# Performance work log

Hardware: AMD Instinct MI355X
Metric: run time of the kernel (lower is better)

## Reference

```python
import math
import jax, jax.numpy as jnp
import numpy as np

B, T, D, M, S = 2, 4096, 1024, 256, 8
BEAM = 4
TAU = 1.0


def setup_inputs() -> dict:
    key = jax.random.key(0)
    ks = jax.random.split(key, 24)
    std = 0.02
    inp = {
        "mu": jax.random.normal(ks[0], (B, T, D), jnp.float32),
        "lam": jax.random.uniform(ks[1], (B, T, D), jnp.float32),
        "pi": jax.random.uniform(ks[2], (B, T, 7), jnp.float32),
        "pi_write": jax.random.uniform(ks[3], (B, T, 1), jnp.float32),
        "Wq": jax.random.normal(ks[4], (M, D), jnp.float32) * std,
        "bq": jnp.zeros((M,), jnp.float32),
        "Wk": jax.random.normal(ks[5], (M, D), jnp.float32) * std,
        "bk": jnp.zeros((M,), jnp.float32),
        "Wv": jax.random.normal(ks[6], (M, D), jnp.float32) * std,
        "bv": jnp.zeros((M,), jnp.float32),
        "Wo": jax.random.normal(ks[7], (D, M), jnp.float32) * std,
        "bo": jnp.zeros((D,), jnp.float32),
        "Ws1": jax.random.normal(ks[8], (256, 2 * D + 7), jnp.float32) * std,
        "bs1": jnp.zeros((256,), jnp.float32),
        "Ws2": jax.random.normal(ks[9], (1, 256), jnp.float32) * std,
        "bs2": jnp.zeros((1,), jnp.float32),
        "Wsr": jax.random.normal(ks[10], (M, M), jnp.float32) * std,
        "bsr": jnp.zeros((M,), jnp.float32),
        "scratch_init": jax.random.normal(ks[11], (1, S, M), jnp.float32) * 0.02,
        "gate": jnp.float32(-5.0),
    }
    return inp


def _build_tree(k, v, w):
    """Causal binary tree of weighted span summaries. Level 0 = leaves."""
    levels = [(k, v, w)]
    while k.shape[1] > 1:
        n = k.shape[1]
        if n % 2 == 1:
            pad = ((0, 0), (0, 1), (0, 0))
            k = jnp.pad(k, pad); v = jnp.pad(v, pad); w = jnp.pad(w, pad)
        k1, k2 = k[:, 0::2], k[:, 1::2]
        v1, v2 = v[:, 0::2], v[:, 1::2]
        w1, w2 = w[:, 0::2], w[:, 1::2]
        tw = w1 + w2 + 1e-8
        k = (w1 * k1 + w2 * k2) / tw
        v = (w1 * v1 + w2 * v2) / tw
        w = tw
        levels.append((k, v, w))
    return levels


def _retrieve_at_level(q, keys, values, beam):
    Bq, Tq, Mq = q.shape
    n = keys.shape[1]
    scores = jnp.einsum('btm,bnm->btn', q, keys) / math.sqrt(Mq)
    if n <= Tq:  # causal: query i may only see slot j <= i
        mask = jnp.arange(n)[None, :] > jnp.arange(Tq)[:, None]
        scores = jnp.where(mask[None], -jnp.inf, scores)
    kk = min(beam, n)
    if n > kk:
        vals, idx = jax.lax.top_k(scores, kk)           # (B,T,k)
        p = jax.nn.softmax(vals, axis=-1)               # == softmax of scattered sparse scores
        v_sel = jnp.take_along_axis(values[:, None], idx[..., None], axis=2)  # (B,T,k,M)
        return jnp.einsum('btk,btkm->btm', p, v_sel)
    attn = jax.nn.softmax(scores, axis=-1)
    return jnp.einsum('btn,bnm->btm', attn, values)


def reference(mu, lam, pi, pi_write, Wq, bq, Wk, bk, Wv, bv, Wo, bo,
              Ws1, bs1, Ws2, bs2, Wsr, bsr, scratch_init, gate):
    # ---- write: build causal tree from detached keys/values ----
    mu_d = jax.lax.stop_gradient(mu)
    w0 = jax.lax.stop_gradient(pi_write)                # (B,T,1)
    k = mu_d @ Wk.T + bk
    v = mu_d @ Wv.T + bv
    tree = _build_tree(k, v, w0)

    # ---- read ----
    q = mu @ Wq.T + bq                                  # (B,T,M)
    log_var = -jnp.log(jnp.clip(lam, 1e-6))
    si = jnp.concatenate([mu, log_var, pi], axis=-1)    # (B,T,2D+7)
    h = si @ Ws1.T + bs1
    h = h * jax.nn.sigmoid(h)                           # SiLU
    s = jax.nn.sigmoid((h @ Ws2.T + bs2)[..., 0])       # (B,T)

    scratch = jnp.broadcast_to(scratch_init, (mu.shape[0], S, M))
    sq = q @ Wsr.T + bsr
    sattn = jax.nn.softmax(jnp.einsum('btm,bsm->bts', sq, scratch) / math.sqrt(M), axis=-1)
    scratch_ctx = jnp.einsum('bts,bsm->btm', sattn, scratch)

    level_ctx = [_retrieve_at_level(q, lk, lv, BEAM) for (lk, lv, _) in tree]
    level_stack = jnp.stack(level_ctx, axis=2)          # (B,T,L,M)
    L = level_stack.shape[2]
    level_idx = jnp.arange(L, dtype=mu.dtype)
    s_scaled = s[..., None] * (L - 1)                   # (B,T,1)
    kappa = jnp.exp(-0.5 * ((level_idx - s_scaled) / TAU) ** 2)
    kappa = kappa / jnp.clip(kappa.sum(axis=-1, keepdims=True), 1e-8)
    tree_ctx = jnp.einsum('btl,btlm->btm', kappa, level_stack)

    blend = s[..., None]
    combined = (1.0 - blend) * tree_ctx + blend * scratch_ctx
    out = combined @ Wo.T + bo
    return jax.nn.sigmoid(gate) * out                   # (B,T,D)
```

## Files before the change

### kernel.cpp

```cpp
#include <hip/hip_runtime.h>
#include <math.h>

#define TT 4096
#define BB 2
#define MMDIM 256
#define RTOT 8192
#define NSLICE 39

typedef __attribute__((ext_vector_type(8))) short short8_t;
typedef __attribute__((ext_vector_type(4))) float f32x4;

__device__ __forceinline__ unsigned short f2bf(float x)
{
    unsigned u = __float_as_uint(x);
    u += 0x7fffu + ((u >> 16) & 1u);
    return (unsigned short)(u >> 16);
}

__global__ __launch_bounds__(256) void gemm_qk(
    const float* __restrict__ mu, const float* __restrict__ Wq,
    const float* __restrict__ bq, const float* __restrict__ Wk,
    const float* __restrict__ bk, float* __restrict__ q_, float* __restrict__ k_,
    unsigned short* __restrict__ qkh, unsigned short* __restrict__ qkl)
{
    __shared__ float As[2][8][68];
    __shared__ float Ws[2][8][132];
    const int tid = threadIdx.x;
    const int tx = tid & 15;
    const int ty = tid >> 4;
    const int r0 = blockIdx.x * 64;
    const int c0 = blockIdx.y * 128;
    const bool isq = (c0 < 256);

    const float* W = isq ? (Wq + (size_t)c0 * 1024)
                         : (Wk + (size_t)(c0 - 256) * 1024);
    const float* bias = isq ? (bq + c0) : (bk + (c0 - 256));

    const bool isA = (tid < 128);
    const int sArow = tid >> 1, sAk = (tid & 1) * 4;
    const int sWrow = tid >> 1, sWk = (tid & 1) * 4;

    float acc[4][8] = {};
    float4 rA, rW;

    if (isA) rA = *(const float4*)&mu[(size_t)(r0 + sArow) * 1024 + sAk];
    rW = *(const float4*)&W[(size_t)sWrow * 1024 + sWk];
    if (isA) {
        As[0][sAk + 0][sArow] = rA.x; As[0][sAk + 1][sArow] = rA.y;
        As[0][sAk + 2][sArow] = rA.z; As[0][sAk + 3][sArow] = rA.w;
    }
    Ws[0][sWk + 0][sWrow] = rW.x; Ws[0][sWk + 1][sWrow] = rW.y;
    Ws[0][sWk + 2][sWrow] = rW.z; Ws[0][sWk + 3][sWrow] = rW.w;
    __syncthreads();

    int buf = 0;
    for (int k0 = 0; k0 < 1024; k0 += 8) {
        const bool has = (k0 + 8 < 1024);
        if (has) {
            if (isA) rA = *(const float4*)&mu[(size_t)(r0 + sArow) * 1024 + k0 + 8 + sAk];
            rW = *(const float4*)&W[(size_t)sWrow * 1024 + k0 + 8 + sWk];
        }
        #pragma unroll
        for (int kk = 0; kk < 8; ++kk) {
            float4 a  = *(const float4*)&As[buf][kk][ty * 4];
            float4 b0 = *(const float4*)&Ws[buf][kk][tx * 8];
            float4 b1 = *(const float4*)&Ws[buf][kk][tx * 8 + 4];
            float av[4] = {a.x, a.y, a.z, a.w};
            float bv[8] = {b0.x, b0.y, b0.z, b0.w, b1.x, b1.y, b1.z, b1.w};
            #pragma unroll
            for (int i = 0; i < 4; ++i)
                #pragma unroll
                for (int j = 0; j < 8; ++j)
                    acc[i][j] += av[i] * bv[j];
        }
        if (has) {
            int nb = buf ^ 1;
            if (isA) {
                As[nb][sAk + 0][sArow] = rA.x; As[nb][sAk + 1][sArow] = rA.y;
                As[nb][sAk + 2][sArow] = rA.z; As[nb][sAk + 3][sArow] = rA.w;
            }
            Ws[nb][sWk + 0][sWrow] = rW.x; Ws[nb][sWk + 1][sWrow] = rW.y;
            Ws[nb][sWk + 2][sWrow] = rW.z; Ws[nb][sWk + 3][sWrow] = rW.w;
        }
        __syncthreads();
        buf ^= 1;
    }

    const int lcol = (c0 & 255) + tx * 8;
    #pragma unroll
    for (int i = 0; i < 4; ++i) {
        int row = r0 + ty * 4 + i;
        float o[8];
        #pragma unroll
        for (int j = 0; j < 8; ++j) o[j] = acc[i][j] + bias[tx * 8 + j];
        float* dst = isq ? &q_[(size_t)row * MMDIM + lcol]
                         : &k_[(size_t)row * MMDIM + lcol];
        *(float4*)dst       = make_float4(o[0], o[1], o[2], o[3]);
        *(float4*)(dst + 4) = make_float4(o[4], o[5], o[6], o[7]);
        size_t srow = isq ? (size_t)row : (size_t)(RTOT + row);
        short8_t sh, sl;
        #pragma unroll
        for (int j = 0; j < 8; ++j) {
            unsigned short h = f2bf(o[j]);
            sh[j] = (short)h;
            sl[j] = (short)f2bf(o[j] - __uint_as_float((unsigned)h << 16));
        }
        *(short8_t*)&qkh[srow * MMDIM + lcol] = sh;
        *(short8_t*)&qkl[srow * MMDIM + lcol] = sl;
    }
}

__device__ __forceinline__ void split4(const float* src, unsigned short* hi,
                                       unsigned short* lo, int i)
{
    float4 x = ((const float4*)src)[i];
    ushort4 h, l;
    h.x = f2bf(x.x); l.x = f2bf(x.x - __uint_as_float((unsigned)h.x << 16));
    h.y = f2bf(x.y); l.y = f2bf(x.y - __uint_as_float((unsigned)h.y << 16));
    h.z = f2bf(x.z); l.z = f2bf(x.z - __uint_as_float((unsigned)h.z << 16));
    h.w = f2bf(x.w); l.w = f2bf(x.w - __uint_as_float((unsigned)h.w << 16));
    ((ushort4*)hi)[i] = h;
    ((ushort4*)lo)[i] = l;
}

__global__ __launch_bounds__(256) void split_weights(
    const float* __restrict__ Ws1, const float* __restrict__ Wv,
    const float* __restrict__ Wsr, const float* __restrict__ Wo,
    unsigned short* __restrict__ w1h, unsigned short* __restrict__ w1l,
    unsigned short* __restrict__ wvh, unsigned short* __restrict__ wvl,
    unsigned short* __restrict__ wsrh, unsigned short* __restrict__ wsrl,
    unsigned short* __restrict__ woh, unsigned short* __restrict__ wol)
{
    const int bid = blockIdx.x;
    const int tid = threadIdx.x;
    if (bid < 256) {
        int r = bid;
        for (int c = tid; c < 2112; c += 256) {
            float v = (c < 2055) ? Ws1[(size_t)r * 2055 + c] : 0.f;
            unsigned short h = f2bf(v);
            w1h[(size_t)r * 2112 + c] = h;
            w1l[(size_t)r * 2112 + c] = f2bf(v - __uint_as_float((unsigned)h << 16));
        }
    } else if (bid < 512) {
        split4(Wv, wvh, wvl, (bid - 256) * 256 + tid);
    } else if (bid < 576) {
        split4(Wsr, wsrh, wsrl, (bid - 512) * 256 + tid);
    } else {
        split4(Wo, woh, wol, (bid - 576) * 256 + tid);
    }
}

template<int ASRC, int WITH_GATE>
__global__ __launch_bounds__(256) void gemm_mfma(
    const float* __restrict__ A, const float* __restrict__ lam,
    const float* __restrict__ pi,
    const unsigned short* __restrict__ Wh, const unsigned short* __restrict__ Wl,
    const float* __restrict__ bias, const float* __restrict__ gate,
    float* __restrict__ C, int K, int N)
{
    __shared__ unsigned short Ah[64][72], Al[64][72];
    __shared__ unsigned short Bh[128][72], Bl[128][72];
    const int tid = threadIdx.x;
    const int lane = tid & 63;
    const int wv = tid >> 6;
    const int r0 = blockIdx.x * 64;
    const int c0 = blockIdx.y * 128;

    f32x4 acc0[8] = {}, acc1[8] = {}, acc2[8] = {};

    const int arow = wv * 16 + (lane & 15);
    const int koff = (lane >> 4) * 8;

    for (int kc = 0; kc < K; kc += 64) {
        #pragma unroll
        for (int i = 0; i < 2; ++i) {
            int g = tid + i * 256;
            int row = g >> 3, gq = g & 7;
            float x[8];
            if (ASRC == 0) {
                float4 v0 = *(const float4*)&A[(size_t)(r0 + row) * K + kc + gq * 8];
                float4 v1 = *(const float4*)&A[(size_t)(r0 + row) * K + kc + gq * 8 + 4];
                x[0] = v0.x; x[1] = v0.y; x[2] = v0.z; x[3] = v0.w;
                x[4] = v1.x; x[5] = v1.y; x[6] = v1.z; x[7] = v1.w;
            } else {
                #pragma unroll
                for (int e = 0; e < 8; ++e) {
                    int c = kc + gq * 8 + e;
                    float val;
                    if (c < 1024)      val = A[(size_t)(r0 + row) * 1024 + c];
                    else if (c < 2048) val = -logf(fmaxf(lam[(size_t)(r0 + row) * 1024 + (c - 1024)], 1e-6f));
                    else if (c < 2055) val = pi[(size_t)(r0 + row) * 7 + (c - 2048)];
                    else               val = 0.f;
                    x[e] = val;
                }
            }
            short8_t sh, sl;
            #pragma unroll
            for (int e = 0; e < 8; ++e) {
                unsigned short h = f2bf(x[e]);
                sh[e] = (short)h;
                sl[e] = (short)f2bf(x[e] - __uint_as_float((unsigned)h << 16));
            }
            *(short8_t*)&Ah[row][gq * 8] = sh;
            *(short8_t*)&Al[row][gq * 8] = sl;
        }
        #pragma unroll
        for (int i = 0; i < 4; ++i) {
            int g = tid + i * 256;
            int row = g >> 3, gq = g & 7;
            *(short8_t*)&Bh[row][gq * 8] = *(const short8_t*)&Wh[(size_t)(c0 + row) * K + kc + gq * 8];
            *(short8_t*)&Bl[row][gq * 8] = *(const short8_t*)&Wl[(size_t)(c0 + row) * K + kc + gq * 8];
        }
        __syncthreads();
        #pragma unroll
        for (int kt = 0; kt < 2; ++kt) {
            short8_t afh = *(const short8_t*)&Ah[arow][kt * 32 + koff];
            short8_t afl = *(const short8_t*)&Al[arow][kt * 32 + koff];
            #pragma unroll
            for (int ct = 0; ct < 8; ++ct) {
                short8_t bh = *(const short8_t*)&Bh[ct * 16 + (lane & 15)][kt * 32 + koff];
                short8_t bl = *(const short8_t*)&Bl[ct * 16 + (lane & 15)][kt * 32 + koff];
                acc0[ct] = __builtin_amdgcn_mfma_f32_16x16x32_bf16(afh, bh, acc0[ct], 0, 0, 0);
                acc1[ct] = __builtin_amdgcn_mfma_f32_16x16x32_bf16(afl, bh, acc1[ct], 0, 0, 0);
                acc2[ct] = __builtin_amdgcn_mfma_f32_16x16x32_bf16(afh, bl, acc2[ct], 0, 0, 0);
            }
        }
        __syncthreads();
    }

    float g = 1.f;
    if (WITH_GATE) g = 1.f / (1.f + expf(-gate[0]));
    #pragma unroll
    for (int ct = 0; ct < 8; ++ct) {
        int col = c0 + ct * 16 + (lane & 15);
        float b = bias[col];
        #pragma unroll
        for (int r = 0; r < 4; ++r) {
            int row = r0 + wv * 16 + (lane >> 4) * 4 + r;
            C[(size_t)row * N + col] = (acc0[ct][r] + acc1[ct][r] + acc2[ct][r] + b) * g;
        }
    }
}

__global__ __launch_bounds__(256) void s_scratch_kernel(
    const float* __restrict__ h, const float* __restrict__ Ws2,
    const float* __restrict__ bs2, const float* __restrict__ sq,
    const float* __restrict__ scr, float* __restrict__ kap,
    float* __restrict__ ctx)
{
    const int tid = threadIdx.x;
    const int wave = tid >> 6, lane = tid & 63;
    const int t = blockIdx.x * 4 + wave;

    float4 hv = *(const float4*)&h[(size_t)t * MMDIM + lane * 4];
    float4 wv = *(const float4*)&Ws2[lane * 4];
    float p = 0.f;
    p += (hv.x / (1.f + expf(-hv.x))) * wv.x;
    p += (hv.y / (1.f + expf(-hv.y))) * wv.y;
    p += (hv.z / (1.f + expf(-hv.z))) * wv.z;
    p += (hv.w / (1.f + expf(-hv.w))) * wv.w;
    #pragma unroll
    for (int o = 32; o; o >>= 1) p += __shfl_xor(p, o);

    float z = p + bs2[0];
    float s = 1.f / (1.f + expf(-z));
    float c = s * 12.f;
    float Z = 0.f;
    #pragma unroll
    for (int l = 0; l < 13; ++l) {
        float d = (float)l - c;
        Z += expf(-0.5f * d * d);
    }
    Z = fmaxf(Z, 1e-8f);
    if (lane < 13) {
        float d = (float)lane - c;
        kap[(size_t)t * 16 + lane] = (1.f - s) * expf(-0.5f * d * d) / Z;
    }

    float4 qv = *(const float4*)&sq[(size_t)t * MMDIM + lane * 4];
    float4 fr[8];
    float sc[8];
    #pragma unroll
    for (int ss = 0; ss < 8; ++ss) {
        fr[ss] = *(const float4*)&scr[ss * MMDIM + lane * 4];
        sc[ss] = qv.x * fr[ss].x + qv.y * fr[ss].y + qv.z * fr[ss].z + qv.w * fr[ss].w;
    }
    #pragma unroll
    for (int ss = 0; ss < 8; ++ss) {
        #pragma unroll
        for (int o = 32; o; o >>= 1) sc[ss] += __shfl_xor(sc[ss], o);
        sc[ss] *= 0.0625f;
    }
    float mx = sc[0];
    #pragma unroll
    for (int ss = 1; ss < 8; ++ss) mx = fmaxf(mx, sc[ss]);
    float sum = 0.f;
    #pragma unroll
    for (int ss = 0; ss < 8; ++ss) { sc[ss] = expf(sc[ss] - mx); sum += sc[ss]; }
    float inv = 1.f / sum;
    float4 o = {0, 0, 0, 0};
    #pragma unroll
    for (int ss = 0; ss < 8; ++ss) {
        float pp = sc[ss] * inv;
        o.x += pp * fr[ss].x; o.y += pp * fr[ss].y;
        o.z += pp * fr[ss].z; o.w += pp * fr[ss].w;
    }
    o.x *= s; o.y *= s; o.z *= s; o.w *= s;
    *(float4*)&ctx[(size_t)t * MMDIM + lane * 4] = o;
}

__global__ __launch_bounds__(256) void wtree_kernel(
    const float* __restrict__ pw, float* __restrict__ wtree)
{
    __shared__ float wa[4096];
    __shared__ float wb2[2048];
    const int b = blockIdx.x;
    const int tid = threadIdx.x;
    for (int t = tid; t < 4096; t += 256) wa[t] = pw[b * 4096 + t];
    __syncthreads();
    int n = 4096, lvl = 1;
    float* cur = wa; float* nxt = wb2;
    while (n > 1) {
        int nout = n >> 1;
        int off = TT - (8192 >> lvl);
        for (int j = tid; j < nout; j += 256) {
            float t = cur[2 * j] + cur[2 * j + 1] + 1e-8f;
            nxt[j] = t;
            wtree[b * 4095 + off + j] = t;
        }
        __syncthreads();
        float* tmp = cur; cur = nxt; nxt = tmp;
        n = nout; ++lvl;
    }
}

__global__ __launch_bounds__(256) void tree_all(
    const float* __restrict__ kleaf, const float* __restrict__ vleaf,
    const float* __restrict__ pw, const float* __restrict__ wtree,
    float* __restrict__ kt_, float* __restrict__ vt_,
    unsigned short* __restrict__ kth, unsigned short* __restrict__ ktl)
{
    __shared__ float kb[254][64];
    __shared__ float vb[254][64];
    const int tid = threadIdx.x;
    const int g  = blockIdx.x >> 2;
    const int mc = blockIdx.x & 3;
    const int b  = blockIdx.y;
    const int wb = b * 4095;

    for (int idx = tid; idx < 128 * 64; idx += 256) {
        int j = idx >> 6, m = idx & 63;
        size_t gi = ((size_t)b * TT + g * 128 + j) * MMDIM + mc * 64 + m;
        kb[j][m] = kleaf[gi];
        vb[j][m] = vleaf[gi];
    }
    __syncthreads();

    int pb = 0, cb = 128;
    for (int l = 1; l <= 6; ++l) {
        int nloc = 64 >> (l - 1);
        int offl = TT - (8192 >> l);
        int gbase = g * nloc;
        for (int idx = tid; idx < nloc * 64; idx += 256) {
            int j = idx >> 6, m = idx & 63;
            float w1, w2;
            if (l == 1) {
                w1 = pw[b * 4096 + (gbase + j) * 2];
                w2 = pw[b * 4096 + (gbase + j) * 2 + 1];
            } else {
                int offm1 = TT - (8192 >> (l - 1));
                w1 = wtree[wb + offm1 + (gbase + j) * 2];
                w2 = wtree[wb + offm1 + (gbase + j) * 2 + 1];
            }
            float tw = wtree[wb + offl + gbase + j];
            float kvv = (w1 * kb[pb + 2 * j][m] + w2 * kb[pb + 2 * j + 1][m]) / tw;
            float vvv = (w1 * vb[pb + 2 * j][m] + w2 * vb[pb + 2 * j + 1][m]) / tw;
            kb[cb + j][m] = kvv;
            vb[cb + j][m] = vvv;
            size_t go = (size_t)(wb + offl + gbase + j) * MMDIM + mc * 64 + m;
            kt_[go] = kvv;
            vt_[go] = vvv;
            unsigned short hh = f2bf(kvv);
            kth[go] = hh;
            ktl[go] = f2bf(kvv - __uint_as_float((unsigned)hh << 16));
        }
        __syncthreads();
        pb = cb; cb += nloc;
    }
}

__global__ __launch_bounds__(256) void tree_deep(
    float* __restrict__ kt_, float* __restrict__ vt_,
    const float* __restrict__ wtree,
    unsigned short* __restrict__ kth, unsigned short* __restrict__ ktl)
{
    __shared__ float kb[128][68];
    __shared__ float vb[128][68];
    const int tid = threadIdx.x;
    const int mc = blockIdx.x;
    const int b = blockIdx.y;
    const int wb = b * 4095;

    for (int idx = tid; idx < 64 * 64; idx += 256) {
        int j = idx >> 6, m = idx & 63;
        size_t gi = (size_t)(wb + 3968 + j) * MMDIM + mc * 64 + m;
        kb[j][m] = kt_[gi];
        vb[j][m] = vt_[gi];
    }
    __syncthreads();

    int pb = 0;
    for (int l = 7; l <= 12; ++l) {
        int nout = 4096 >> l;
        int cb = 128 - (128 >> (l - 6));
        int offm1 = TT - (8192 >> (l - 1));
        int offl  = TT - (8192 >> l);
        for (int idx = tid; idx < nout * 64; idx += 256) {
            int j = idx >> 6, m = idx & 63;
            float w1 = wtree[wb + offm1 + 2 * j];
            float w2 = wtree[wb + offm1 + 2 * j + 1];
            float tw = wtree[wb + offl + j];
            float kvv = (w1 * kb[pb + 2 * j][m] + w2 * kb[pb + 2 * j + 1][m]) / tw;
            float vvv = (w1 * vb[pb + 2 * j][m] + w2 * vb[pb + 2 * j + 1][m]) / tw;
            kb[cb + j][m] = kvv;
            vb[cb + j][m] = vvv;
            size_t go = (size_t)(wb + offl + j) * MMDIM + mc * 64 + m;
            kt_[go] = kvv;
            vt_[go] = vvv;
            unsigned short hh = f2bf(kvv);
            kth[go] = hh;
            ktl[go] = f2bf(kvv - __uint_as_float((unsigned)hh << 16));
        }
        __syncthreads();
        pb = cb;
    }
}

__device__ __forceinline__ unsigned long long pack_key(float v, int col)
{
    unsigned u = __float_as_uint(v);
    u ^= ((unsigned)((int)u >> 31)) | 0x80000000u;
    return ((unsigned long long)u << 32) | (unsigned)(~col);
}

__device__ __forceinline__ void unpack_key(unsigned long long k, float& v, int& col)
{
    unsigned u = (unsigned)(k >> 32);
    u ^= (u & 0x80000000u) ? 0x80000000u : 0xFFFFFFFFu;
    v = __uint_as_float(u);
    col = (int)(~(unsigned)k);
}

__device__ __forceinline__ unsigned long long shfl_xor_u64(unsigned long long v, int off)
{
    int lo = __shfl_xor((int)(unsigned)v, off);
    int hi = __shfl_xor((int)(v >> 32), off);
    return ((unsigned long long)(unsigned)hi << 32) | (unsigned)lo;
}

__device__ __forceinline__ void ins4u(unsigned long long k, unsigned long long t[4])
{
    if (k <= t[3]) return;
    t[3] = k;
    if (t[3] > t[2]) { unsigned long long x = t[2]; t[2] = t[3]; t[3] = x; }
    if (t[2] > t[1]) { unsigned long long x = t[1]; t[1] = t[2]; t[2] = x; }
    if (t[1] > t[0]) { unsigned long long x = t[0]; t[0] = t[1]; t[1] = x; }
}

__device__ __forceinline__ void ins5u(unsigned long long k, unsigned long long t[5])
{
    if (k <= t[4]) return;
    t[4] = k;
    if (t[4] > t[3]) { unsigned long long x = t[3]; t[3] = t[4]; t[4] = x; }
    if (t[3] > t[2]) { unsigned long long x = t[2]; t[2] = t[3]; t[3] = x; }
    if (t[2] > t[1]) { unsigned long long x = t[1]; t[1] = t[2]; t[2] = x; }
    if (t[1] > t[0]) { unsigned long long x = t[0]; t[0] = t[1]; t[1] = x; }
}

__device__ __forceinline__ bool beats(float v, int id, float v2, int id2)
{
    return (v > v2) || (v == v2 && id < id2);
}

__device__ __forceinline__ void ins5(float v, int id, float tv[5], int ti[5])
{
    if (!beats(v, id, tv[4], ti[4])) return;
    tv[4] = v; ti[4] = id;
    #pragma unroll
    for (int s = 4; s > 0; --s) {
        if (beats(tv[s], ti[s], tv[s - 1], ti[s - 1])) {
            float fv = tv[s]; tv[s] = tv[s - 1]; tv[s - 1] = fv;
            int iv = ti[s]; ti[s] = ti[s - 1]; ti[s - 1] = iv;
        }
    }
}

__device__ __forceinline__ void slice_map(int sid, int& level, int& c0)
{
    if (sid < 16)      { level = 0; c0 = sid << 8; }
    else if (sid < 24) { level = 1; c0 = (sid - 16) << 8; }
    else if (sid < 28) { level = 2; c0 = (sid - 24) << 8; }
    else if (sid < 30) { level = 3; c0 = (sid - 28) << 8; }
    else               { level = sid - 26; c0 = 0; }
}

__global__ __launch_bounds__(256) void topk_mfma(
    const unsigned short* __restrict__ qkh, const unsigned short* __restrict__ qkl,
    const unsigned short* __restrict__ kth, const unsigned short* __restrict__ ktl,
    float2* __restrict__ topw)
{
    __shared__ unsigned short kbh[32][264];
    __shared__ unsigned short kbl[32][264];

    const int tid = threadIdx.x;
    const int lane = tid & 63;
    const int wv = tid >> 6;
    const int r0 = blockIdx.x * 64;
    const int sid = blockIdx.y;
    const int b = r0 >> 12;
    const int t0 = r0 & 4095;

    int level, c0b;
    slice_map(sid, level, c0b);
    const int n = TT >> level;
    const int nv = min(min(n, t0 + 64), c0b + 256);

    if (c0b >= nv) {
        if (tid < 64) {
            float2 e = make_float2(-INFINITY, __int_as_float(0x7fffffff));
            #pragma unroll
            for (int s = 0; s < 5; ++s)
                topw[(size_t)(sid * 5 + s) * RTOT + r0 + tid] = e;
        }
        return;
    }

    const unsigned short* Kh;
    const unsigned short* Kl;
    if (level == 0) {
        Kh = qkh + (size_t)RTOT * MMDIM + (size_t)b * TT * MMDIM;
        Kl = qkl + (size_t)RTOT * MMDIM + (size_t)b * TT * MMDIM;
    } else {
        size_t off = (size_t)b * 4095 + (TT - (8192 >> level));
        Kh = kth + off * MMDIM;
        Kl = ktl + off * MMDIM;
    }

    const int arow = r0 + wv * 16 + (lane & 15);
    const int koff = (lane >> 4) * 8;
    short8_t ah[8], al[8];
    #pragma unroll
    for (int kt = 0; kt < 8; ++kt) {
        ah[kt] = *(const short8_t*)(qkh + (size_t)arow * MMDIM + kt * 32 + koff);
        al[kt] = *(const short8_t*)(qkl + (size_t)arow * MMDIM + kt * 32 + koff);
    }

    unsigned long long tk[4][4] = {};
    const int trow0 = t0 + wv * 16 + (lane >> 4) * 4;

    const int scol = tid >> 3;
    const int kseg = (tid & 7) * 32;

    for (int c0 = c0b; c0 < nv; c0 += 32) {
        {
            int cc = min(c0 + scol, n - 1);
            const unsigned short* gh = Kh + (size_t)cc * MMDIM + kseg;
            const unsigned short* gl = Kl + (size_t)cc * MMDIM + kseg;
            #pragma unroll
            for (int i = 0; i < 4; ++i) {
                *(short8_t*)&kbh[scol][kseg + i * 8] = *(const short8_t*)(gh + i * 8);
                *(short8_t*)&kbl[scol][kseg + i * 8] = *(const short8_t*)(gl + i * 8);
            }
        }
        __syncthreads();

        #pragma unroll
        for (int ct = 0; ct < 2; ++ct) {
            f32x4 a0 = {0.f, 0.f, 0.f, 0.f};
            f32x4 a1 = {0.f, 0.f, 0.f, 0.f};
            f32x4 a2 = {0.f, 0.f, 0.f, 0.f};
            const int bc = ct * 16 + (lane & 15);
            #pragma unroll
            for (int kt = 0; kt < 8; ++kt) {
                short8_t bh = *(const short8_t*)&kbh[bc][kt * 32 + koff];
                short8_t bl = *(const short8_t*)&kbl[bc][kt * 32 + koff];
                a0 = __builtin_amdgcn_mfma_f32_16x16x32_bf16(ah[kt], bh, a0, 0, 0, 0);
                a1 = __builtin_amdgcn_mfma_f32_16x16x32_bf16(al[kt], bh, a1, 0, 0, 0);
                a2 = __builtin_amdgcn_mfma_f32_16x16x32_bf16(ah[kt], bl, a2, 0, 0, 0);
            }
            const int col = c0 + bc;
            #pragma unroll
            for (int r = 0; r < 4; ++r) {
                float sc = (a0[r] + a1[r] + a2[r]) * 0.0625f;
                unsigned long long key =
                    (col <= trow0 + r && col < n) ? pack_key(sc, col) : 0ull;
                if (__any(key > tk[r][3])) ins4u(key, tk[r]);
            }
        }
        __syncthreads();
    }

    #pragma unroll
    for (int r = 0; r < 4; ++r) {
        unsigned long long k5[5];
        #pragma unroll
        for (int s = 0; s < 4; ++s) k5[s] = tk[r][s];
        k5[4] = 0ull;
        #pragma unroll
        for (int pass = 0; pass < 4; ++pass) {
            int off = 1 << pass;
            unsigned long long o[5];
            #pragma unroll
            for (int s = 0; s < 5; ++s) o[s] = shfl_xor_u64(k5[s], off);
            #pragma unroll
            for (int s = 0; s < 5; ++s) ins5u(o[s], k5);
        }
        if ((lane & 15) == 0) {
            int row = r0 + wv * 16 + (lane >> 4) * 4 + r;
            #pragma unroll
            for (int s = 0; s < 5; ++s) {
                float2 e;
                if (k5[s] == 0ull) {
                    e = make_float2(-INFINITY, __int_as_float(0x7fffffff));
                } else {
                    float v; int c;
                    unpack_key(k5[s], v, c);
                    e = make_float2(v, __int_as_float(c));
                }
                topw[(size_t)(sid * 5 + s) * RTOT + row] = e;
            }
        }
    }
}

__global__ __launch_bounds__(256) void merge_gather(
    const float2* __restrict__ topw, const float* __restrict__ q,
    const float* __restrict__ kl0, const float* __restrict__ ktf,
    const float* __restrict__ vl0, const float* __restrict__ vtree,
    const float* __restrict__ kap, float* __restrict__ ctx)
{
    const int tid = threadIdx.x;
    const int lane = tid & 63;
    const int wv = __builtin_amdgcn_readfirstlane(tid >> 6);
    const int row = blockIdx.x * 4 + wv;
    const int b = row >> 12;

    float cr[4] = {0, 0, 0, 0};
    const float4 q4 = *(const float4*)&q[(size_t)row * MMDIM + lane * 4];

    for (int l = 0; l <= 12; ++l) {
        int s0, cnt;
        if (l == 0)      { s0 = 0;  cnt = 16; }
        else if (l == 1) { s0 = 16; cnt = 8; }
        else if (l == 2) { s0 = 24; cnt = 4; }
        else if (l == 3) { s0 = 28; cnt = 2; }
        else             { s0 = 26 + l; cnt = 1; }

        float tv[5]; int ti[5];
        #pragma unroll
        for (int s = 0; s < 5; ++s) { tv[s] = -INFINITY; ti[s] = 0x7fffffff; }
        for (int sl = 0; sl < cnt; ++sl) {
            #pragma unroll
            for (int s = 0; s < 5; ++s) {
                float2 e = topw[(size_t)((s0 + sl) * 5 + s) * RTOT + row];
                if (e.x > -INFINITY) ins5(e.x, __float_as_int(e.y), tv, ti);
            }
        }

        const float* Kf = (l == 0)
            ? kl0 + (size_t)b * TT * MMDIM
            : ktf + ((size_t)b * 4095 + (TT - (8192 >> l))) * MMDIM;

        bool ambig = (l <= 9) && (tv[3] - tv[4] < 1e-4f);
        if (ambig) {
            float rv[5]; int ri[5];
            #pragma unroll
            for (int s = 0; s < 5; ++s) { rv[s] = -INFINITY; ri[s] = 0x7fffffff; }
            for (int sl = 0; sl < cnt; ++sl) {
                #pragma unroll
                for (int s = 0; s < 5; ++s) {
                    float2 e = topw[(size_t)((s0 + sl) * 5 + s) * RTOT + row];
                    if (e.x > -INFINITY) {
                        int idx = __float_as_int(e.y);
                        float4 k4 = *(const float4*)&Kf[(size_t)idx * MMDIM + lane * 4];
                        float p = q4.x * k4.x + q4.y * k4.y + q4.z * k4.z + q4.w * k4.w;
                        #pragma unroll
                        for (int o = 32; o; o >>= 1) p += __shfl_xor(p, o);
                        ins5(p * 0.0625f, idx, rv, ri);
                    }
                }
            }
            #pragma unroll
            for (int s = 0; s < 5; ++s) { tv[s] = rv[s]; ti[s] = ri[s]; }
        }

        float m0 = tv[0];
        float e0 = expf(tv[0] - m0);
        float e1 = expf(tv[1] - m0);
        float e2 = expf(tv[2] - m0);
        float e3 = expf(tv[3] - m0);
        float sum = e0 + e1 + e2 + e3;
        float kp = kap[(size_t)row * 16 + l];
        float scl = kp / sum;
        float ps[4] = {e0 * scl, e1 * scl, e2 * scl, e3 * scl};

        const float* Vb = (l == 0)
            ? vl0 + (size_t)b * TT * MMDIM
            : vtree + ((size_t)b * 4095 + (TT - (8192 >> l))) * MMDIM;

        #pragma unroll
        for (int s = 0; s < 4; ++s) {
            if (ps[s] > 0.f) {
                float4 vv = *(const float4*)&Vb[(size_t)ti[s] * MMDIM + lane * 4];
                cr[0] += ps[s] * vv.x; cr[1] += ps[s] * vv.y;
                cr[2] += ps[s] * vv.z; cr[3] += ps[s] * vv.w;
            }
        }
    }

    float* cp = ctx + (size_t)row * MMDIM + lane * 4;
    float4 c = *(float4*)cp;
    c.x += cr[0]; c.y += cr[1]; c.z += cr[2]; c.w += cr[3];
    *(float4*)cp = c;
}

extern "C" void kernel_launch(void* const* d_in, const int* in_sizes, int n_in,
                              void* d_out, int out_size, void* d_ws, size_t ws_size,
                              hipStream_t stream)
{
    const float* mu  = (const float*)d_in[0];
    const float* lam = (const float*)d_in[1];
    const float* pi  = (const float*)d_in[2];
    const float* pw  = (const float*)d_in[3];
    const float* Wq  = (const float*)d_in[4];
    const float* bq  = (const float*)d_in[5];
    const float* Wk  = (const float*)d_in[6];
    const float* bk  = (const float*)d_in[7];
    const float* Wv  = (const float*)d_in[8];
    const float* bv  = (const float*)d_in[9];
    const float* Wo  = (const float*)d_in[10];
    const float* bo  = (const float*)d_in[11];
    const float* Ws1 = (const float*)d_in[12];
    const float* bs1 = (const float*)d_in[13];
    const float* Ws2 = (const float*)d_in[14];
    const float* bs2 = (const float*)d_in[15];
    const float* Wsr = (const float*)d_in[16];
    const float* bsr = (const float*)d_in[17];
    const float* scr = (const float*)d_in[18];
    const float* gate = (const float*)d_in[19];
    float* out = (float*)d_out;

    float* w = (float*)d_ws;
    const size_t RM = (size_t)RTOT * MMDIM;
    float* q_   = w;  w += RM;
    float* k_   = w;  w += RM;
    float* v_   = w;  w += RM;
    float* h_   = w;  w += RM;
    float* sq_  = w;  w += RM;
    float* ctx_ = w;  w += RM;
    float* sb_  = w;  w += RTOT;
    float* kap_ = w;  w += (size_t)RTOT * 16;
    float* kt_  = w;  w += (size_t)BB * 4095 * MMDIM;
    float* vt_  = w;  w += (size_t)BB * 4095 * MMDIM;
    float* wtree_ = w; w += (size_t)BB * 4095;
    unsigned short* qkh_ = (unsigned short*)w;  w += RM;
    unsigned short* qkl_ = (unsigned short*)w;  w += RM;
    unsigned short* kth_ = (unsigned short*)w;  w += (size_t)BB * 4095 * MMDIM / 2;
    unsigned short* ktl_ = (unsigned short*)w;  w += (size_t)BB * 4095 * MMDIM / 2;
    float2* topw = (float2*)w;  w += (size_t)NSLICE * 5 * RTOT * 2;
    unsigned short* w1h_ = (unsigned short*)w;  w += (size_t)256 * 2112 / 2;
    unsigned short* w1l_ = (unsigned short*)w;  w += (size_t)256 * 2112 / 2;
    unsigned short* wvh_ = (unsigned short*)w;  w += (size_t)256 * 1024 / 2;
    unsigned short* wvl_ = (unsigned short*)w;  w += (size_t)256 * 1024 / 2;
    unsigned short* wsrh_ = (unsigned short*)w; w += (size_t)256 * 256 / 2;
    unsigned short* wsrl_ = (unsigned short*)w; w += (size_t)256 * 256 / 2;
    unsigned short* woh_ = (unsigned short*)w;  w += (size_t)1024 * 256 / 2;
    unsigned short* wol_ = (unsigned short*)w;  w += (size_t)1024 * 256 / 2;
    (void)sb_;

    split_weights<<<832, 256, 0, stream>>>(Ws1, Wv, Wsr, Wo,
                                           w1h_, w1l_, wvh_, wvl_,
                                           wsrh_, wsrl_, woh_, wol_);

    gemm_qk<<<dim3(128, 4), 256, 0, stream>>>(mu, Wq, bq, Wk, bk,
                                              q_, k_, qkh_, qkl_);
    gemm_mfma<0, 0><<<dim3(128, 2), 256, 0, stream>>>(mu, nullptr, nullptr, wvh_, wvl_,
                                                      bv, nullptr, v_, 1024, 256);
    gemm_mfma<1, 0><<<dim3(128, 2), 256, 0, stream>>>(mu, lam, pi, w1h_, w1l_,
                                                      bs1, nullptr, h_, 2112, 256);
    gemm_mfma<0, 0><<<dim3(128, 2), 256, 0, stream>>>(q_, nullptr, nullptr, wsrh_, wsrl_,
                                                      bsr, nullptr, sq_, 256, 256);
    s_scratch_kernel<<<2048, 256, 0, stream>>>(h_, Ws2, bs2, sq_, scr, kap_, ctx_);

    wtree_kernel<<<BB, 256, 0, stream>>>(pw, wtree_);
    tree_all<<<dim3(128, BB), 256, 0, stream>>>(k_, v_, pw, wtree_, kt_, vt_,
                                                kth_, ktl_);
    tree_deep<<<dim3(4, BB), 256, 0, stream>>>(kt_, vt_, wtree_, kth_, ktl_);

    topk_mfma<<<dim3(128, NSLICE), 256, 0, stream>>>(qkh_, qkl_, kth_, ktl_, topw);
    merge_gather<<<2048, 256, 0, stream>>>(topw, q_, k_, kt_, v_, vt_, kap_, ctx_);
    gemm_mfma<0, 1><<<dim3(128, 8), 256, 0, stream>>>(ctx_, nullptr, nullptr, woh_, wol_,
                                                      bo, gate, out, 256, 1024);
}
```

Baseline: 735.1 us.

## Fuse QK GEMM with weight splitting, merge V/H GEMMs, compute tree weights in-block

Folds the weight bf16 hi/lo splitting into the Q/K projection kernel as extra blocks, retiled to 128 threads with an 8x8 per-thread micro-tile. Merges the V and H MFMA GEMMs into one launch selected by blockIdx.y. Drops the separate tree-weight kernel: tree_all and tree_deep now build the per-level weights in shared memory, and only level-6 weights pass between them. This removes several kernel launches and serial small-grid work, at the cost of larger per-thread register use in the QK GEMM and mixed block roles.

```diff
diff --git a/kernel.cpp b/kernel.cpp
--- a/kernel.cpp
+++ b/kernel.cpp
@@ -15,99 +15,6 @@
     unsigned u = __float_as_uint(x);
     u += 0x7fffu + ((u >> 16) & 1u);
     return (unsigned short)(u >> 16);
-}
-
-__global__ __launch_bounds__(256) void gemm_qk(
-    const float* __restrict__ mu, const float* __restrict__ Wq,
-    const float* __restrict__ bq, const float* __restrict__ Wk,
-    const float* __restrict__ bk, float* __restrict__ q_, float* __restrict__ k_,
-    unsigned short* __restrict__ qkh, unsigned short* __restrict__ qkl)
-{
-    __shared__ float As[2][8][68];
-    __shared__ float Ws[2][8][132];
-    const int tid = threadIdx.x;
-    const int tx = tid & 15;
-    const int ty = tid >> 4;
-    const int r0 = blockIdx.x * 64;
-    const int c0 = blockIdx.y * 128;
-    const bool isq = (c0 < 256);
-
-    const float* W = isq ? (Wq + (size_t)c0 * 1024)
-                         : (Wk + (size_t)(c0 - 256) * 1024);
-    const float* bias = isq ? (bq + c0) : (bk + (c0 - 256));
-
-    const bool isA = (tid < 128);
-    const int sArow = tid >> 1, sAk = (tid & 1) * 4;
-    const int sWrow = tid >> 1, sWk = (tid & 1) * 4;
-
-    float acc[4][8] = {};
-    float4 rA, rW;
-
-    if (isA) rA = *(const float4*)&mu[(size_t)(r0 + sArow) * 1024 + sAk];
-    rW = *(const float4*)&W[(size_t)sWrow * 1024 + sWk];
-    if (isA) {
-        As[0][sAk + 0][sArow] = rA.x; As[0][sAk + 1][sArow] = rA.y;
-        As[0][sAk + 2][sArow] = rA.z; As[0][sAk + 3][sArow] = rA.w;
-    }
-    Ws[0][sWk + 0][sWrow] = rW.x; Ws[0][sWk + 1][sWrow] = rW.y;
-    Ws[0][sWk + 2][sWrow] = rW.z; Ws[0][sWk + 3][sWrow] = rW.w;
-    __syncthreads();
-
-    int buf = 0;
-    for (int k0 = 0; k0 < 1024; k0 += 8) {
-        const bool has = (k0 + 8 < 1024);
-        if (has) {
-            if (isA) rA = *(const float4*)&mu[(size_t)(r0 + sArow) * 1024 + k0 + 8 + sAk];
-            rW = *(const float4*)&W[(size_t)sWrow * 1024 + k0 + 8 + sWk];
-        }
-        #pragma unroll
-        for (int kk = 0; kk < 8; ++kk) {
-            float4 a  = *(const float4*)&As[buf][kk][ty * 4];
-            float4 b0 = *(const float4*)&Ws[buf][kk][tx * 8];
-            float4 b1 = *(const float4*)&Ws[buf][kk][tx * 8 + 4];
-            float av[4] = {a.x, a.y, a.z, a.w};
-            float bv[8] = {b0.x, b0.y, b0.z, b0.w, b1.x, b1.y, b1.z, b1.w};
-            #pragma unroll
-            for (int i = 0; i < 4; ++i)
-                #pragma unroll
-                for (int j = 0; j < 8; ++j)
-                    acc[i][j] += av[i] * bv[j];
-        }
-        if (has) {
-            int nb = buf ^ 1;
-            if (isA) {
-                As[nb][sAk + 0][sArow] = rA.x; As[nb][sAk + 1][sArow] = rA.y;
-                As[nb][sAk + 2][sArow] = rA.z; As[nb][sAk + 3][sArow] = rA.w;
-            }
-            Ws[nb][sWk + 0][sWrow] = rW.x; Ws[nb][sWk + 1][sWrow] = rW.y;
-            Ws[nb][sWk + 2][sWrow] = rW.z; Ws[nb][sWk + 3][sWrow] = rW.w;
-        }
-        __syncthreads();
-        buf ^= 1;
-    }
-
-    const int lcol = (c0 & 255) + tx * 8;
-    #pragma unroll
-    for (int i = 0; i < 4; ++i) {
-        int row = r0 + ty * 4 + i;
-        float o[8];
-        #pragma unroll
-        for (int j = 0; j < 8; ++j) o[j] = acc[i][j] + bias[tx * 8 + j];
-        float* dst = isq ? &q_[(size_t)row * MMDIM + lcol]
-                         : &k_[(size_t)row * MMDIM + lcol];
-        *(float4*)dst       = make_float4(o[0], o[1], o[2], o[3]);
-        *(float4*)(dst + 4) = make_float4(o[4], o[5], o[6], o[7]);
-        size_t srow = isq ? (size_t)row : (size_t)(RTOT + row);
-        short8_t sh, sl;
-        #pragma unroll
-        for (int j = 0; j < 8; ++j) {
-            unsigned short h = f2bf(o[j]);
-            sh[j] = (short)h;
-            sl[j] = (short)f2bf(o[j] - __uint_as_float((unsigned)h << 16));
-        }
-        *(short8_t*)&qkh[srow * MMDIM + lcol] = sh;
-        *(short8_t*)&qkl[srow * MMDIM + lcol] = sl;
-    }
 }
 
 __device__ __forceinline__ void split4(const float* src, unsigned short* hi,
@@ -123,7 +30,11 @@
     ((ushort4*)lo)[i] = l;
 }
 
-__global__ __launch_bounds__(256) void split_weights(
+__global__ __launch_bounds__(128) void qk_split(
+    const float* __restrict__ mu, const float* __restrict__ Wq,
+    const float* __restrict__ bq, const float* __restrict__ Wk,
+    const float* __restrict__ bk, float* __restrict__ q_, float* __restrict__ k_,
+    unsigned short* __restrict__ qkh, unsigned short* __restrict__ qkl,
     const float* __restrict__ Ws1, const float* __restrict__ Wv,
     const float* __restrict__ Wsr, const float* __restrict__ Wo,
     unsigned short* __restrict__ w1h, unsigned short* __restrict__ w1l,
@@ -131,40 +42,140 @@
     unsigned short* __restrict__ wsrh, unsigned short* __restrict__ wsrl,
     unsigned short* __restrict__ woh, unsigned short* __restrict__ wol)
 {
+    __shared__ float As[2][8][68];
+    __shared__ float Ws[2][8][132];
     const int bid = blockIdx.x;
     const int tid = threadIdx.x;
-    if (bid < 256) {
-        int r = bid;
-        for (int c = tid; c < 2112; c += 256) {
-            float v = (c < 2055) ? Ws1[(size_t)r * 2055 + c] : 0.f;
-            unsigned short h = f2bf(v);
-            w1h[(size_t)r * 2112 + c] = h;
-            w1l[(size_t)r * 2112 + c] = f2bf(v - __uint_as_float((unsigned)h << 16));
-        }
-    } else if (bid < 512) {
-        split4(Wv, wvh, wvl, (bid - 256) * 256 + tid);
-    } else if (bid < 576) {
-        split4(Wsr, wsrh, wsrl, (bid - 512) * 256 + tid);
-    } else {
-        split4(Wo, woh, wol, (bid - 576) * 256 + tid);
+
+    if (bid >= 512) {
+        const int sid = bid - 512;
+        if (sid < 256) {
+            int r = sid;
+            for (int c = tid; c < 2112; c += 128) {
+                float v = (c < 2055) ? Ws1[(size_t)r * 2055 + c] : 0.f;
+                unsigned short h = f2bf(v);
+                w1h[(size_t)r * 2112 + c] = h;
+                w1l[(size_t)r * 2112 + c] = f2bf(v - __uint_as_float((unsigned)h << 16));
+            }
+        } else if (sid < 768) {
+            split4(Wv, wvh, wvl, (sid - 256) * 128 + tid);
+        } else if (sid < 896) {
+            split4(Wsr, wsrh, wsrl, (sid - 768) * 128 + tid);
+        } else {
+            split4(Wo, woh, wol, (sid - 896) * 128 + tid);
+        }
+        return;
+    }
+
+    const int bx = bid >> 2;
+    const int by = bid & 3;
+    const int r0 = bx * 64;
+    const int c0 = by * 128;
+    const bool isq = (c0 < 256);
+
+    const float* W = isq ? (Wq + (size_t)c0 * 1024)
+                         : (Wk + (size_t)(c0 - 256) * 1024);
+    const float* bias = isq ? (bq + (c0 & 255)) : (bk + (c0 & 255));
+
+    const int tx = tid & 15;
+    const int ty = tid >> 4;
+    const int sArow = tid >> 1, sAk = (tid & 1) * 4;
+    const int sWcol = tid;
+
+    float acc[8][8] = {};
+    float4 rA, rW0, rW1;
+
+    rA  = *(const float4*)&mu[(size_t)(r0 + sArow) * 1024 + sAk];
+    rW0 = *(const float4*)&W[(size_t)sWcol * 1024 + 0];
+    rW1 = *(const float4*)&W[(size_t)sWcol * 1024 + 4];
+    As[0][sAk + 0][sArow] = rA.x; As[0][sAk + 1][sArow] = rA.y;
+    As[0][sAk + 2][sArow] = rA.z; As[0][sAk + 3][sArow] = rA.w;
+    Ws[0][0][sWcol] = rW0.x; Ws[0][1][sWcol] = rW0.y;
+    Ws[0][2][sWcol] = rW0.z; Ws[0][3][sWcol] = rW0.w;
+    Ws[0][4][sWcol] = rW1.x; Ws[0][5][sWcol] = rW1.y;
+    Ws[0][6][sWcol] = rW1.z; Ws[0][7][sWcol] = rW1.w;
+    __syncthreads();
+
+    int buf = 0;
+    for (int k0 = 0; k0 < 1024; k0 += 8) {
+        const bool has = (k0 + 8 < 1024);
+        if (has) {
+            rA  = *(const float4*)&mu[(size_t)(r0 + sArow) * 1024 + k0 + 8 + sAk];
+            rW0 = *(const float4*)&W[(size_t)sWcol * 1024 + k0 + 8];
+            rW1 = *(const float4*)&W[(size_t)sWcol * 1024 + k0 + 12];
+        }
+        #pragma unroll
+        for (int kk = 0; kk < 8; ++kk) {
+            float4 a0 = *(const float4*)&As[buf][kk][ty * 4];
+            float4 a1 = *(const float4*)&As[buf][kk][32 + ty * 4];
+            float4 b0 = *(const float4*)&Ws[buf][kk][tx * 4];
+            float4 b1 = *(const float4*)&Ws[buf][kk][64 + tx * 4];
+            float av[8] = {a0.x, a0.y, a0.z, a0.w, a1.x, a1.y, a1.z, a1.w};
+            float bv[8] = {b0.x, b0.y, b0.z, b0.w, b1.x, b1.y, b1.z, b1.w};
+            #pragma unroll
+            for (int i = 0; i < 8; ++i)
+                #pragma unroll
+                for (int j = 0; j < 8; ++j)
+                    acc[i][j] += av[i] * bv[j];
+        }
+        if (has) {
+            int nb = buf ^ 1;
+            As[nb][sAk + 0][sArow] = rA.x; As[nb][sAk + 1][sArow] = rA.y;
+            As[nb][sAk + 2][sArow] = rA.z; As[nb][sAk + 3][sArow] = rA.w;
+            Ws[nb][0][sWcol] = rW0.x; Ws[nb][1][sWcol] = rW0.y;
+            Ws[nb][2][sWcol] = rW0.z; Ws[nb][3][sWcol] = rW0.w;
+            Ws[nb][4][sWcol] = rW1.x; Ws[nb][5][sWcol] = rW1.y;
+            Ws[nb][6][sWcol] = rW1.z; Ws[nb][7][sWcol] = rW1.w;
+        }
+        __syncthreads();
+        buf ^= 1;
+    }
+
+    const int lc0 = (c0 & 255) + tx * 4;
+    const int lc1 = lc0 + 64;
+    #pragma unroll
+    for (int i = 0; i < 8; ++i) {
+        int row = r0 + ((i < 4) ? (ty * 4 + i) : (32 + ty * 4 + i - 4));
+        float o[8];
+        #pragma unroll
+        for (int j = 0; j < 4; ++j) o[j]     = acc[i][j]     + bias[tx * 4 + j];
+        #pragma unroll
+        for (int j = 0; j < 4; ++j) o[4 + j] = acc[i][4 + j] + bias[64 + tx * 4 + j];
+        float* dst = isq ? q_ : k_;
+        *(float4*)&dst[(size_t)row * MMDIM + lc0] = make_float4(o[0], o[1], o[2], o[3]);
+        *(float4*)&dst[(size_t)row * MMDIM + lc1] = make_float4(o[4], o[5], o[6], o[7]);
+        size_t srow = isq ? (size_t)row : (size_t)(RTOT + row);
+        ushort4 h0, l0, h1, l1;
+        h0.x = f2bf(o[0]); l0.x = f2bf(o[0] - __uint_as_float((unsigned)h0.x << 16));
+        h0.y = f2bf(o[1]); l0.y = f2bf(o[1] - __uint_as_float((unsigned)h0.y << 16));
+        h0.z = f2bf(o[2]); l0.z = f2bf(o[2] - __uint_as_float((unsigned)h0.z << 16));
+        h0.w = f2bf(o[3]); l0.w = f2bf(o[3] - __uint_as_float((unsigned)h0.w << 16));
+        h1.x = f2bf(o[4]); l1.x = f2bf(o[4] - __uint_as_float((unsigned)h1.x << 16));
+        h1.y = f2bf(o[5]); l1.y = f2bf(o[5] - __uint_as_float((unsigned)h1.y << 16));
+        h1.z = f2bf(o[6]); l1.z = f2bf(o[6] - __uint_as_float((unsigned)h1.z << 16));
+        h1.w = f2bf(o[7]); l1.w = f2bf(o[7] - __uint_as_float((unsigned)h1.w << 16));
+        *(ushort4*)&qkh[srow * MMDIM + lc0] = h0;
+        *(ushort4*)&qkl[srow * MMDIM + lc0] = l0;
+        *(ushort4*)&qkh[srow * MMDIM + lc1] = h1;
+        *(ushort4*)&qkl[srow * MMDIM + lc1] = l1;
     }
 }
 
 template<int ASRC, int WITH_GATE>
-__global__ __launch_bounds__(256) void gemm_mfma(
+__device__ __forceinline__ void gemm_mfma_body(
+    unsigned short (*Ah)[72], unsigned short (*Al)[72],
+    unsigned short (*Bh)[72], unsigned short (*Bl)[72],
     const float* __restrict__ A, const float* __restrict__ lam,
     const float* __restrict__ pi,
     const unsigned short* __restrict__ Wh, const unsigned short* __restrict__ Wl,
     const float* __restrict__ bias, const float* __restrict__ gate,
-    float* __restrict__ C, int K, int N)
-{
-    __shared__ unsigned short Ah[64][72], Al[64][72];
-    __shared__ unsigned short Bh[128][72], Bl[128][72];
+    float* __restrict__ C, int K, int N, int bx, int by)
+{
     const int tid = threadIdx.x;
     const int lane = tid & 63;
     const int wv = tid >> 6;
-    const int r0 = blockIdx.x * 64;
-    const int c0 = blockIdx.y * 128;
+    const int r0 = bx * 64;
+    const int c0 = by * 128;
 
     f32x4 acc0[8] = {}, acc1[8] = {}, acc2[8] = {};
 
@@ -242,6 +253,39 @@
     }
 }
 
+template<int ASRC, int WITH_GATE>
+__global__ __launch_bounds__(256) void gemm_mfma(
+    const float* __restrict__ A, const float* __restrict__ lam,
+    const float* __restrict__ pi,
+    const unsigned short* __restrict__ Wh, const unsigned short* __restrict__ Wl,
+    const float* __restrict__ bias, const float* __restrict__ gate,
+    float* __restrict__ C, int K, int N)
+{
+    __shared__ unsigned short Ah[64][72], Al[64][72];
+    __shared__ unsigned short Bh[128][72], Bl[128][72];
+    gemm_mfma_body<ASRC, WITH_GATE>(Ah, Al, Bh, Bl, A, lam, pi, Wh, Wl,
+                                    bias, gate, C, K, N, blockIdx.x, blockIdx.y);
+}
+
+__global__ __launch_bounds__(256) void gemm_vh(
+    const float* __restrict__ mu, const float* __restrict__ lam,
+    const float* __restrict__ pi,
+    const unsigned short* __restrict__ wvh, const unsigned short* __restrict__ wvl,
+    const float* __restrict__ bv,
+    const unsigned short* __restrict__ w1h, const unsigned short* __restrict__ w1l,
+    const float* __restrict__ bs1,
+    float* __restrict__ v_, float* __restrict__ h_)
+{
+    __shared__ unsigned short Ah[64][72], Al[64][72];
+    __shared__ unsigned short Bh[128][72], Bl[128][72];
+    if (blockIdx.y < 2)
+        gemm_mfma_body<0, 0>(Ah, Al, Bh, Bl, mu, nullptr, nullptr, wvh, wvl,
+                             bv, nullptr, v_, 1024, 256, blockIdx.x, blockIdx.y);
+    else
+        gemm_mfma_body<1, 0>(Ah, Al, Bh, Bl, mu, lam, pi, w1h, w1l,
+                             bs1, nullptr, h_, 2112, 256, blockIdx.x, blockIdx.y - 2);
+}
+
 __global__ __launch_bounds__(256) void s_scratch_kernel(
     const float* __restrict__ h, const float* __restrict__ Ws2,
     const float* __restrict__ bs2, const float* __restrict__ sq,
@@ -309,39 +353,15 @@
     *(float4*)&ctx[(size_t)t * MMDIM + lane * 4] = o;
 }
 
-__global__ __launch_bounds__(256) void wtree_kernel(
-    const float* __restrict__ pw, float* __restrict__ wtree)
-{
-    __shared__ float wa[4096];
-    __shared__ float wb2[2048];
-    const int b = blockIdx.x;
-    const int tid = threadIdx.x;
-    for (int t = tid; t < 4096; t += 256) wa[t] = pw[b * 4096 + t];
-    __syncthreads();
-    int n = 4096, lvl = 1;
-    float* cur = wa; float* nxt = wb2;
-    while (n > 1) {
-        int nout = n >> 1;
-        int off = TT - (8192 >> lvl);
-        for (int j = tid; j < nout; j += 256) {
-            float t = cur[2 * j] + cur[2 * j + 1] + 1e-8f;
-            nxt[j] = t;
-            wtree[b * 4095 + off + j] = t;
-        }
-        __syncthreads();
-        float* tmp = cur; cur = nxt; nxt = tmp;
-        n = nout; ++lvl;
-    }
-}
-
 __global__ __launch_bounds__(256) void tree_all(
     const float* __restrict__ kleaf, const float* __restrict__ vleaf,
-    const float* __restrict__ pw, const float* __restrict__ wtree,
+    const float* __restrict__ pw, float* __restrict__ wl6,
     float* __restrict__ kt_, float* __restrict__ vt_,
     unsigned short* __restrict__ kth, unsigned short* __restrict__ ktl)
 {
     __shared__ float kb[254][64];
     __shared__ float vb[254][64];
+    __shared__ float wl[254];
     const int tid = threadIdx.x;
     const int g  = blockIdx.x >> 2;
     const int mc = blockIdx.x & 3;
@@ -354,25 +374,22 @@
         kb[j][m] = kleaf[gi];
         vb[j][m] = vleaf[gi];
     }
+    if (tid < 128) wl[tid] = pw[b * 4096 + g * 128 + tid];
     __syncthreads();
 
     int pb = 0, cb = 128;
     for (int l = 1; l <= 6; ++l) {
-        int nloc = 64 >> (l - 1);
+        int nloc = 128 >> l;
         int offl = TT - (8192 >> l);
         int gbase = g * nloc;
+        if (tid < nloc)
+            wl[cb + tid] = wl[pb + 2 * tid] + wl[pb + 2 * tid + 1] + 1e-8f;
+        __syncthreads();
         for (int idx = tid; idx < nloc * 64; idx += 256) {
             int j = idx >> 6, m = idx & 63;
-            float w1, w2;
-            if (l == 1) {
-                w1 = pw[b * 4096 + (gbase + j) * 2];
-                w2 = pw[b * 4096 + (gbase + j) * 2 + 1];
-            } else {
-                int offm1 = TT - (8192 >> (l - 1));
-                w1 = wtree[wb + offm1 + (gbase + j) * 2];
-                w2 = wtree[wb + offm1 + (gbase + j) * 2 + 1];
-            }
-            float tw = wtree[wb + offl + gbase + j];
+            float w1 = wl[pb + 2 * j];
+            float w2 = wl[pb + 2 * j + 1];
+            float tw = wl[cb + j];
             float kvv = (w1 * kb[pb + 2 * j][m] + w2 * kb[pb + 2 * j + 1][m]) / tw;
             float vvv = (w1 * vb[pb + 2 * j][m] + w2 * vb[pb + 2 * j + 1][m]) / tw;
             kb[cb + j][m] = kvv;
@@ -387,15 +404,17 @@
         __syncthreads();
         pb = cb; cb += nloc;
     }
+    if (mc == 0 && tid < 2) wl6[b * 64 + g * 2 + tid] = wl[pb + tid];
 }
 
 __global__ __launch_bounds__(256) void tree_deep(
     float* __restrict__ kt_, float* __restrict__ vt_,
-    const float* __restrict__ wtree,
+    const float* __restrict__ wl6,
     unsigned short* __restrict__ kth, unsigned short* __restrict__ ktl)
 {
     __shared__ float kb[128][68];
     __shared__ float vb[128][68];
+    __shared__ float wl[127];
     const int tid = threadIdx.x;
     const int mc = blockIdx.x;
     const int b = blockIdx.y;
@@ -407,19 +426,23 @@
         kb[j][m] = kt_[gi];
         vb[j][m] = vt_[gi];
     }
+    if (tid < 64) wl[tid] = wl6[b * 64 + tid];
     __syncthreads();
 
     int pb = 0;
+    int pbw = 0, cbw = 64;
     for (int l = 7; l <= 12; ++l) {
         int nout = 4096 >> l;
         int cb = 128 - (128 >> (l - 6));
-        int offm1 = TT - (8192 >> (l - 1));
-        int offl  = TT - (8192 >> l);
+        int offl = TT - (8192 >> l);
+        if (tid < nout)
+            wl[cbw + tid] = wl[pbw + 2 * tid] + wl[pbw + 2 * tid + 1] + 1e-8f;
+        __syncthreads();
         for (int idx = tid; idx < nout * 64; idx += 256) {
             int j = idx >> 6, m = idx & 63;
-            float w1 = wtree[wb + offm1 + 2 * j];
-            float w2 = wtree[wb + offm1 + 2 * j + 1];
-            float tw = wtree[wb + offl + j];
+            float w1 = wl[pbw + 2 * j];
+            float w2 = wl[pbw + 2 * j + 1];
+            float tw = wl[cbw + j];
             float kvv = (w1 * kb[pb + 2 * j][m] + w2 * kb[pb + 2 * j + 1][m]) / tw;
             float vvv = (w1 * vb[pb + 2 * j][m] + w2 * vb[pb + 2 * j + 1][m]) / tw;
             kb[cb + j][m] = kvv;
@@ -433,6 +456,7 @@
         }
         __syncthreads();
         pb = cb;
+        pbw = cbw; cbw += nout;
     }
 }
 
@@ -762,7 +786,7 @@
     float* kap_ = w;  w += (size_t)RTOT * 16;
     float* kt_  = w;  w += (size_t)BB * 4095 * MMDIM;
     float* vt_  = w;  w += (size_t)BB * 4095 * MMDIM;
-    float* wtree_ = w; w += (size_t)BB * 4095;
+    float* wl6_ = w;  w += (size_t)BB * 4095;
     unsigned short* qkh_ = (unsigned short*)w;  w += RM;
     unsigned short* qkl_ = (unsigned short*)w;  w += RM;
     unsigned short* kth_ = (unsigned short*)w;  w += (size_t)BB * 4095 * MMDIM / 2;
@@ -778,24 +802,20 @@
     unsigned short* wol_ = (unsigned short*)w;  w += (size_t)1024 * 256 / 2;
     (void)sb_;
 
-    split_weights<<<832, 256, 0, stream>>>(Ws1, Wv, Wsr, Wo,
-                                           w1h_, w1l_, wvh_, wvl_,
-                                           wsrh_, wsrl_, woh_, wol_);
-
-    gemm_qk<<<dim3(128, 4), 256, 0, stream>>>(mu, Wq, bq, Wk, bk,
-                                              q_, k_, qkh_, qkl_);
-    gemm_mfma<0, 0><<<dim3(128, 2), 256, 0, stream>>>(mu, nullptr, nullptr, wvh_, wvl_,
-                                                      bv, nullptr, v_, 1024, 256);
-    gemm_mfma<1, 0><<<dim3(128, 2), 256, 0, stream>>>(mu, lam, pi, w1h_, w1l_,
-                                                      bs1, nullptr, h_, 2112, 256);
+    qk_split<<<1920, 128, 0, stream>>>(mu, Wq, bq, Wk, bk, q_, k_, qkh_, qkl_,
+                                       Ws1, Wv, Wsr, Wo,
+                                       w1h_, w1l_, wvh_, wvl_,
+                                       wsrh_, wsrl_, woh_, wol_);
+
+    gemm_vh<<<dim3(128, 4), 256, 0, stream>>>(mu, lam, pi, wvh_, wvl_, bv,
+                                              w1h_, w1l_, bs1, v_, h_);
     gemm_mfma<0, 0><<<dim3(128, 2), 256, 0, stream>>>(q_, nullptr, nullptr, wsrh_, wsrl_,
                                                       bsr, nullptr, sq_, 256, 256);
     s_scratch_kernel<<<2048, 256, 0, stream>>>(h_, Ws2, bs2, sq_, scr, kap_, ctx_);
 
-    wtree_kernel<<<BB, 256, 0, stream>>>(pw, wtree_);
-    tree_all<<<dim3(128, BB), 256, 0, stream>>>(k_, v_, pw, wtree_, kt_, vt_,
+    tree_all<<<dim3(128, BB), 256, 0, stream>>>(k_, v_, pw, wl6_, kt_, vt_,
                                                 kth_, ktl_);
-    tree_deep<<<dim3(4, BB), 256, 0, stream>>>(kt_, vt_, wtree_, kth_, ktl_);
+    tree_deep<<<dim3(4, BB), 256, 0, stream>>>(kt_, vt_, wl6_, kth_, ktl_);
 
     topk_mfma<<<dim3(128, NSLICE), 256, 0, stream>>>(qkh_, qkl_, kth_, ktl_, topw);
     merge_gather<<<2048, 256, 0, stream>>>(topw, q_, k_, kt_, v_, vt_, kap_, ctx_);
```

After: 781.8 us. +6.4%, slower.
